# Performance work log

Hardware: AMD Instinct MI355X
Metric: run time of the kernel (lower is better)

The kernel has to match this reference:

```python
import jax, jax.numpy as jnp
import numpy as np

N = 50000      # nodes
E = 800000     # edges
G = 64         # graphs in batch
IN_F, H1, C1, C2, OUT_F = 128, 4, 32, 64, 16
D1 = H1 * C1   # 128, concat output of gat1
EPS = 1e-5
NEG_SLOPE = 0.2


def setup_inputs() -> dict:
    key = jax.random.key(0)
    ks = jax.random.split(key, 16)
    rn = lambda k, shape, s=0.1: jax.random.normal(k, shape, jnp.float32) * s
    inp = {
        'x': jax.random.normal(ks[0], (N, IN_F), jnp.float32),
        'edge_index': jax.random.randint(ks[1], (2, E), 0, N),
        'edge_attr': jax.random.uniform(ks[2], (E, 1), jnp.float32),
        'batch': jnp.sort(jax.random.randint(ks[3], (N,), 0, G)),
        # GATv2 layer 1 (heads=4, concat)
        'Wl1': rn(ks[4], (IN_F, D1)), 'bl1': jnp.zeros((D1,), jnp.float32),
        'Wr1': rn(ks[5], (IN_F, D1)), 'br1': jnp.zeros((D1,), jnp.float32),
        'We1': rn(ks[6], (1, D1)), 'att1': rn(ks[7], (H1, C1)),
        'bias1': jnp.zeros((D1,), jnp.float32),
        # GATv2 layer 2 (heads=1, concat=False)
        'Wl2': rn(ks[8], (D1, C2)), 'bl2': jnp.zeros((C2,), jnp.float32),
        'Wr2': rn(ks[9], (D1, C2)), 'br2': jnp.zeros((C2,), jnp.float32),
        'We2': rn(ks[10], (1, C2)), 'att2': rn(ks[11], (1, C2)),
        'bias2': jnp.zeros((C2,), jnp.float32),
        # batchnorms
        'bn1_gamma': jnp.ones((D1,), jnp.float32), 'bn1_beta': jnp.zeros((D1,), jnp.float32),
        'bn2_gamma': jnp.ones((C2,), jnp.float32), 'bn2_beta': jnp.zeros((C2,), jnp.float32),
        # final linear over [sum|mean|max] pooled features
        'Wlin': rn(ks[12], (3 * C2, OUT_F)), 'blin': jnp.zeros((OUT_F,), jnp.float32),
    }
    return inp


def gatv2(x, src, dst, edge_attr, Wl, bl, Wr, br, We, att, bias, H, C, concat):
    n = x.shape[0]
    xl = (x @ Wl + bl).reshape(n, H, C)          # source transform (lin_l)
    xr = (x @ Wr + br).reshape(n, H, C)          # target transform (lin_r)
    e = (edge_attr @ We).reshape(-1, H, C)       # edge transform (lin_edge)
    m = jax.nn.leaky_relu(xl[src] + xr[dst] + e, NEG_SLOPE)  # [E,H,C]
    alpha = jnp.einsum('ehc,hc->eh', m, att)     # attention logits [E,H]
    amax = jax.ops.segment_max(alpha, dst, num_segments=n)
    amax = jnp.where(jnp.isfinite(amax), amax, 0.0)
    p = jnp.exp(alpha - amax[dst])
    denom = jax.ops.segment_sum(p, dst, num_segments=n)
    a = p / (denom[dst] + 1e-16)                 # per-destination softmax
    out = jax.ops.segment_sum(xl[src] * a[:, :, None], dst, num_segments=n)
    out = out.reshape(n, H * C) if concat else out.mean(axis=1)
    return out + bias


def batchnorm(x, gamma, beta):
    mu = x.mean(axis=0)
    var = x.var(axis=0)  # biased var, as torch BN uses for normalization
    return (x - mu) * jax.lax.rsqrt(var + EPS) * gamma + beta


def reference(x, edge_index, edge_attr, batch,
              Wl1, bl1, Wr1, br1, We1, att1, bias1,
              Wl2, bl2, Wr2, br2, We2, att2, bias2,
              bn1_gamma, bn1_beta, bn2_gamma, bn2_beta,
              Wlin, blin):
    src, dst = edge_index[0], edge_index[1]
    h = jax.nn.relu(gatv2(x, src, dst, edge_attr, Wl1, bl1, Wr1, br1, We1, att1, bias1, H1, C1, True))
    h = batchnorm(h, bn1_gamma, bn1_beta)
    # dropout omitted (eval-mode reference)
    h = jax.nn.relu(gatv2(h, src, dst, edge_attr, Wl2, bl2, Wr2, br2, We2, att2, bias2, 1, C2, False))
    h = batchnorm(h, bn2_gamma, bn2_beta)
    # multi-pool over graphs
    s = jax.ops.segment_sum(h, batch, num_segments=G)
    cnt = jax.ops.segment_sum(jnp.ones((h.shape[0], 1), h.dtype), batch, num_segments=G)
    mean = s / jnp.maximum(cnt, 1.0)
    mx = jax.ops.segment_max(h, batch, num_segments=G)
    feat = jnp.concatenate([s, mean, mx], axis=-1)   # [G, 3*C2]
    return feat @ Wlin + blin
```

## Files before the change

### kernel.cpp

```cpp
#include <hip/hip_runtime.h>
#include <math.h>


typedef __attribute__((ext_vector_type(8))) short short8v;
typedef __attribute__((ext_vector_type(8))) unsigned short ushort8v;
typedef __attribute__((ext_vector_type(4))) unsigned short ushort4v;
typedef __attribute__((ext_vector_type(4))) float f32x4v;

#define BUCKCAP 8192

__device__ __forceinline__ void atomicMaxFloat(float* addr, float val) {
    if (val >= 0.f) atomicMax((int*)addr, __float_as_int(val));
    else            atomicMin((unsigned int*)addr, __float_as_uint(val));
}
__device__ __forceinline__ void atomicMinFloat(float* addr, float val) {
    if (val >= 0.f) atomicMin((int*)addr, __float_as_int(val));
    else            atomicMax((unsigned int*)addr, __float_as_uint(val));
}
__device__ __forceinline__ unsigned short f2bf(float f) {
    unsigned u = __float_as_uint(f);
    unsigned r = u + 0x7FFFu + ((u >> 16) & 1u);
    return (unsigned short)(r >> 16);
}
__device__ __forceinline__ float bf2f(unsigned short h) {
    return __uint_as_float((unsigned)h << 16);
}

__global__ __launch_bounds__(256)
void passA_kernel(const int* __restrict__ esrc_in, const int* __restrict__ edst_in,
                  const float* __restrict__ eattr,
                  const float* __restrict__ Wl1, const float* __restrict__ Wr1,
                  uint2* __restrict__ brec, int* __restrict__ bcur,
                  unsigned short* __restrict__ w1t, float* __restrict__ gsum,
                  float* __restrict__ gmax, float* __restrict__ gmin, int nE) {
    __shared__ unsigned scnt[256];
    __shared__ unsigned sbase[256];
    const int t = threadIdx.x;
    const int e0 = blockIdx.x * 1024;
    scnt[t] = 0;
    __syncthreads();
    unsigned rx[4], ry[4]; unsigned short rk[4];
#pragma unroll
    for (int j = 0; j < 4; ++j) {
        int e = e0 + j * 256 + t;
        if (e < nE) {
            unsigned d = (unsigned)edst_in[e];
            rx[j] = (d << 16) | (unsigned)esrc_in[e];
            ry[j] = __float_as_uint(eattr[e]);
            rk[j] = (unsigned short)atomicAdd(&scnt[d >> 8], 1u);
        }
    }
    __syncthreads();
    sbase[t] = (scnt[t] > 0) ? (unsigned)atomicAdd(&bcur[t], (int)scnt[t]) : 0u;
    __syncthreads();
#pragma unroll
    for (int j = 0; j < 4; ++j) {
        int e = e0 + j * 256 + t;
        if (e < nE) {
            unsigned b = rx[j] >> 24;
            unsigned pos = sbase[b] + rk[j];
            if (pos < BUCKCAP) brec[(size_t)b * BUCKCAP + pos] = make_uint2(rx[j], ry[j]);
        }
    }
    const int gid = blockIdx.x * 256 + t, gstr = gridDim.x * 256;
    for (int j = gid; j < 256 * 128; j += gstr) {
        int col = j >> 7, k = j & 127;
        float w = (col < 128) ? Wl1[k * 128 + col] : Wr1[k * 128 + (col - 128)];
        w1t[j] = f2bf(w);
    }
    for (int j = gid; j < 64 * 64; j += gstr) { gsum[j] = 0.f; gmax[j] = -INFINITY; gmin[j] = INFINITY; }
}

__global__ __launch_bounds__(256)
void passB_kernel(const uint2* __restrict__ brec, const int* __restrict__ bcur,
                  int* __restrict__ rowptr, int* __restrict__ deghist,
                  unsigned* __restrict__ edges, int nN, int nE) {
    __shared__ unsigned cnt[256];
    __shared__ int red[256];
    __shared__ int rp[256];
    __shared__ int lhist[64];
    const int b = blockIdx.x, t = threadIdx.x;
    cnt[t] = 0;
    if (t < 64) lhist[t] = 0;
    red[t] = (t < b) ? bcur[t] : 0;
    __syncthreads();
    for (int off = 128; off; off >>= 1) {
        if (t < off) red[t] += red[t + off];
        __syncthreads();
    }
    const int base = red[0];
    const int n = bcur[b];
    const uint2* r = brec + (size_t)b * BUCKCAP;
    for (int i = t; i < n; i += 256) atomicAdd(&cnt[(r[i].x >> 16) & 255u], 1u);
    __syncthreads();
    const unsigned v = cnt[t];
    const int d = (b << 8) + t;
    if (d < nN) atomicAdd(&lhist[v < 63u ? v : 63u], 1);
    red[t] = (int)v;
    __syncthreads();
    for (int off = 1; off < 256; off <<= 1) {
        int xv = (t >= off) ? red[t - off] : 0;
        __syncthreads();
        red[t] += xv;
        __syncthreads();
    }
    if (t < 64 && lhist[t] > 0) atomicAdd(&deghist[t], lhist[t]);
    rp[t] = base + red[t] - (int)v;
    if (d <= nN) rowptr[d] = rp[t];
    if (b == gridDim.x - 1 && t == 255) rowptr[nN] = nE;
    __syncthreads();
    cnt[t] = 0;
    __syncthreads();
    for (int i = t; i < n; i += 256) {
        uint2 rec = r[i];
        unsigned dlo = (rec.x >> 16) & 255u;
        unsigned rank = atomicAdd(&cnt[dlo], 1u);
        int pos = rp[dlo] + (int)rank;
        edges[pos] = (rec.x & 0xFFFFu) | ((unsigned)f2bf(__uint_as_float(rec.y)) << 16);
    }
}

template <int NO, bool F32IN, bool DOPERM>
__global__ __launch_bounds__(256)
void mfma_transform_kernel(const float* __restrict__ Af, const unsigned short* __restrict__ Ab,
                           const unsigned short* __restrict__ Wt,
                           const float* __restrict__ bL, const float* __restrict__ bR,
                           unsigned short* __restrict__ outL, unsigned short* __restrict__ outR,
                           const int* __restrict__ rowptr, const int* __restrict__ deghist,
                           int* __restrict__ bincur, unsigned short* __restrict__ perm, int M) {
    if constexpr (DOPERM) {
        if ((int)blockIdx.x < (M + 255) / 256) {
            __shared__ int gbase[64];
            __shared__ int lcnt[64];
            __shared__ int lbase[64];
            const int t = threadIdx.x;
            if (t < 64) {
                int v = deghist[t];
                int incl = v;
#pragma unroll
                for (int off = 1; off < 64; off <<= 1) {
                    int u = __shfl_up(incl, off);
                    if (t >= off) incl += u;
                }
                gbase[t] = incl - v;
                lcnt[t] = 0;
            }
            __syncthreads();
            const int dnode = blockIdx.x * 256 + t;
            int bin = 0, myrank = 0;
            if (dnode < M) {
                int deg = rowptr[dnode + 1] - rowptr[dnode];
                bin = deg < 63 ? deg : 63;
                myrank = atomicAdd(&lcnt[bin], 1);
            }
            __syncthreads();
            if (t < 64 && lcnt[t] > 0) lbase[t] = atomicAdd(&bincur[t], lcnt[t]);
            __syncthreads();
            if (dnode < M) perm[gbase[bin] + lbase[bin] + myrank] = (unsigned short)dnode;
        }
    }
    constexpr int NCG = NO / 64;
    const int wid  = (blockIdx.x * blockDim.x + threadIdx.x) >> 6;
    const int lane = threadIdx.x & 63;
    const int rowblk = wid / NCG;
    const int cg     = wid % NCG;
    if (rowblk * 16 >= M) return;
    int r = rowblk * 16 + (lane & 15);
    if (r >= M) r = M - 1;
    const int ko = (lane >> 4) * 8;
    const int cbase = cg * 64;

    f32x4v acc0 = {0.f,0.f,0.f,0.f}, acc1 = acc0, acc2 = acc0, acc3 = acc0;
#pragma unroll
    for (int k0 = 0; k0 < 128; k0 += 32) {
        short8v a;
        if constexpr (F32IN) {
            const float4 f0 = *(const float4*)(Af + (size_t)r * 128 + k0 + ko);
            const float4 f1 = *(const float4*)(Af + (size_t)r * 128 + k0 + ko + 4);
            a[0] = (short)f2bf(f0.x); a[1] = (short)f2bf(f0.y);
            a[2] = (short)f2bf(f0.z); a[3] = (short)f2bf(f0.w);
            a[4] = (short)f2bf(f1.x); a[5] = (short)f2bf(f1.y);
            a[6] = (short)f2bf(f1.z); a[7] = (short)f2bf(f1.w);
        } else {
            a = *(const short8v*)(Ab + (size_t)r * 128 + k0 + ko);
        }
        const unsigned short* wp = Wt + (size_t)(cbase + (lane & 15)) * 128 + k0 + ko;
        short8v b0 = *(const short8v*)(wp);
        short8v b1 = *(const short8v*)(wp + 16 * 128);
        short8v b2 = *(const short8v*)(wp + 32 * 128);
        short8v b3 = *(const short8v*)(wp + 48 * 128);
        acc0 = __builtin_amdgcn_mfma_f32_16x16x32_bf16(a, b0, acc0, 0, 0, 0);
        acc1 = __builtin_amdgcn_mfma_f32_16x16x32_bf16(a, b1, acc1, 0, 0, 0);
        acc2 = __builtin_amdgcn_mfma_f32_16x16x32_bf16(a, b2, acc2, 0, 0, 0);
        acc3 = __builtin_amdgcn_mfma_f32_16x16x32_bf16(a, b3, acc3, 0, 0, 0);
    }

    const int colL  = lane & 15;
    const int rquad = (lane >> 4) * 4;
    f32x4v accs[4] = { acc0, acc1, acc2, acc3 };
#pragma unroll
    for (int c = 0; c < 4; ++c) {
        const int gcol = cbase + c * 16 + colL;
        float bias; unsigned short* outp; int oc;
        if (gcol < NO / 2) { bias = bL[gcol]; outp = outL; oc = gcol; }
        else               { bias = bR[gcol - NO / 2]; outp = outR; oc = gcol - NO / 2; }
#pragma unroll
        for (int j = 0; j < 4; ++j) {
            const int row = rowblk * 16 + rquad + j;
            if (row < M) outp[(size_t)row * (NO / 2) + oc] = f2bf(accs[c][j] + bias);
        }
    }
}

__device__ __forceinline__ float edge_c8(unsigned w, bool act, ushort8v xu,
                                         const float* xrv, const float* wev,
                                         const float* atv, float* xv) {
    const float ea = bf2f((unsigned short)(w >> 16));
    float part = 0.f;
#pragma unroll
    for (int q = 0; q < 8; ++q) {
        xv[q] = bf2f(xu[q]);
        float t = xv[q] + xrv[q] + ea * wev[q];
        t = fmaxf(t, 0.2f * t);
        part += t * atv[q];
    }
    part += __shfl_xor(part, 1);
    part += __shfl_xor(part, 2);
    return act ? __expf(part) : 0.f;
}

__device__ __forceinline__ float edge_c4(unsigned w, bool act, ushort4v xu,
                                         const float* xrv, const float* wev,
                                         const float* atv, float* xv) {
    const float ea = bf2f((unsigned short)(w >> 16));
    float part = 0.f;
#pragma unroll
    for (int q = 0; q < 4; ++q) {
        xv[q] = bf2f(xu[q]);
        float t = xv[q] + xrv[q] + ea * wev[q];
        t = fmaxf(t, 0.2f * t);
        part += t * atv[q];
    }
    part += __shfl_xor(part, 1);
    part += __shfl_xor(part, 2);
    part += __shfl_xor(part, 4);
    part += __shfl_xor(part, 8);
    return act ? __expf(part) : 0.f;
}

__global__ __launch_bounds__(256)
void gather1_kernel(const unsigned short* __restrict__ xl, const unsigned short* __restrict__ xr,
                    const int* __restrict__ rowptr, const unsigned* __restrict__ edges,
                    const unsigned short* __restrict__ perm,
                    const float* __restrict__ We, const float* __restrict__ att,
                    const float* __restrict__ bias, unsigned short* __restrict__ y, int nN) {
    const int lane = threadIdx.x & 63;
    const int sub  = lane >> 4;
    const int sl   = lane & 15;
    const int c0   = sl * 8;
    const int waveg = (blockIdx.x * blockDim.x + threadIdx.x) >> 6;
    const int i = waveg * 4 + sub;
    const bool valid = (i < nN);
    const int n = valid ? (int)perm[i] : 0;

    float xrv[8];
    int ks = 0, ke = 0;
    if (valid) {
        ushort8v xu = *(const ushort8v*)(xr + (size_t)n * 128 + c0);
#pragma unroll
        for (int j = 0; j < 8; ++j) xrv[j] = bf2f(xu[j]);
        ks = rowptr[n]; ke = rowptr[n + 1];
    } else {
#pragma unroll
        for (int j = 0; j < 8; ++j) xrv[j] = 0.f;
    }
    const float4 we0 = *(const float4*)(We + c0);
    const float4 we1 = *(const float4*)(We + c0 + 4);
    const float4 at0 = *(const float4*)(att + c0);
    const float4 at1 = *(const float4*)(att + c0 + 4);
    const float wev[8] = { we0.x, we0.y, we0.z, we0.w, we1.x, we1.y, we1.z, we1.w };
    const float atv[8] = { at0.x, at0.y, at0.z, at0.w, at1.x, at1.y, at1.z, at1.w };

    float d = 0.f, a[8];
#pragma unroll
    for (int j = 0; j < 8; ++j) a[j] = 0.f;

    for (int kb = ks; __any(kb < ke); kb += 16) {
        const unsigned ew = (kb + sl < ke) ? edges[kb + sl] : 0u;
        const int cnt = ke - kb;
        for (int j = 0; j < 16; j += 4) {
            if (!__any(j < cnt)) break;
            const unsigned w0 = __shfl(ew, sub * 16 + j + 0);
            const unsigned w1 = __shfl(ew, sub * 16 + j + 1);
            const unsigned w2 = __shfl(ew, sub * 16 + j + 2);
            const unsigned w3 = __shfl(ew, sub * 16 + j + 3);
            const ushort8v xu0 = *(const ushort8v*)(xl + (size_t)(w0 & 0xFFFFu) * 128 + c0);
            const ushort8v xu1 = *(const ushort8v*)(xl + (size_t)(w1 & 0xFFFFu) * 128 + c0);
            const ushort8v xu2 = *(const ushort8v*)(xl + (size_t)(w2 & 0xFFFFu) * 128 + c0);
            const ushort8v xu3 = *(const ushort8v*)(xl + (size_t)(w3 & 0xFFFFu) * 128 + c0);
            float xva[8], xvb[8];
            const float e0 = edge_c8(w0, j + 0 < cnt, xu0, xrv, wev, atv, xva);
            const float e1 = edge_c8(w1, j + 1 < cnt, xu1, xrv, wev, atv, xvb);
            d += e0 + e1;
#pragma unroll
            for (int q = 0; q < 8; ++q) a[q] += e0 * xva[q] + e1 * xvb[q];
            const float e2 = edge_c8(w2, j + 2 < cnt, xu2, xrv, wev, atv, xva);
            const float e3 = edge_c8(w3, j + 3 < cnt, xu3, xrv, wev, atv, xvb);
            d += e2 + e3;
#pragma unroll
            for (int q = 0; q < 8; ++q) a[q] += e2 * xva[q] + e3 * xvb[q];
        }
    }
    if (valid) {
        const float inv = 1.f / (d + 1e-16f);
        ushort8v o;
#pragma unroll
        for (int j = 0; j < 8; ++j) o[j] = f2bf(fmaxf(a[j] * inv + bias[c0 + j], 0.f));
        *(ushort8v*)(y + (size_t)n * 128 + c0) = o;
    }
}

__global__ __launch_bounds__(256)
void gather2_kernel(const unsigned short* __restrict__ xl, const unsigned short* __restrict__ xr,
                    const int* __restrict__ rowptr, const unsigned* __restrict__ edges,
                    const unsigned short* __restrict__ perm,
                    const float* __restrict__ We, const float* __restrict__ att,
                    const float* __restrict__ bias, float* __restrict__ y, int nN) {
    const int lane = threadIdx.x & 63;
    const int sub  = lane >> 4;
    const int sl   = lane & 15;
    const int c0   = sl * 4;
    const int waveg = (blockIdx.x * blockDim.x + threadIdx.x) >> 6;
    const int i = waveg * 4 + sub;
    const bool valid = (i < nN);
    const int n = valid ? (int)perm[i] : 0;

    float xrv[4];
    int ks = 0, ke = 0;
    if (valid) {
        ushort4v xu = *(const ushort4v*)(xr + (size_t)n * 64 + c0);
#pragma unroll
        for (int j = 0; j < 4; ++j) xrv[j] = bf2f(xu[j]);
        ks = rowptr[n]; ke = rowptr[n + 1];
    } else {
#pragma unroll
        for (int j = 0; j < 4; ++j) xrv[j] = 0.f;
    }
    const float4 wev4 = *(const float4*)(We + c0);
    const float4 atv4 = *(const float4*)(att + c0);
    const float wev[4] = { wev4.x, wev4.y, wev4.z, wev4.w };
    const float atv[4] = { atv4.x, atv4.y, atv4.z, atv4.w };

    float d = 0.f, a[4] = {0.f, 0.f, 0.f, 0.f};
    for (int kb = ks; __any(kb < ke); kb += 16) {
        const unsigned ew = (kb + sl < ke) ? edges[kb + sl] : 0u;
        const int cnt = ke - kb;
        for (int j = 0; j < 16; j += 4) {
            if (!__any(j < cnt)) break;
            const unsigned w0 = __shfl(ew, sub * 16 + j + 0);
            const unsigned w1 = __shfl(ew, sub * 16 + j + 1);
            const unsigned w2 = __shfl(ew, sub * 16 + j + 2);
            const unsigned w3 = __shfl(ew, sub * 16 + j + 3);
            const ushort4v xu0 = *(const ushort4v*)(xl + (size_t)(w0 & 0xFFFFu) * 64 + c0);
            const ushort4v xu1 = *(const ushort4v*)(xl + (size_t)(w1 & 0xFFFFu) * 64 + c0);
            const ushort4v xu2 = *(const ushort4v*)(xl + (size_t)(w2 & 0xFFFFu) * 64 + c0);
            const ushort4v xu3 = *(const ushort4v*)(xl + (size_t)(w3 & 0xFFFFu) * 64 + c0);
            float xva[4], xvb[4];
            const float e0 = edge_c4(w0, j + 0 < cnt, xu0, xrv, wev, atv, xva);
            const float e1 = edge_c4(w1, j + 1 < cnt, xu1, xrv, wev, atv, xvb);
            d += e0 + e1;
#pragma unroll
            for (int q = 0; q < 4; ++q) a[q] += e0 * xva[q] + e1 * xvb[q];
            const float e2 = edge_c4(w2, j + 2 < cnt, xu2, xrv, wev, atv, xva);
            const float e3 = edge_c4(w3, j + 3 < cnt, xu3, xrv, wev, atv, xvb);
            d += e2 + e3;
#pragma unroll
            for (int q = 0; q < 4; ++q) a[q] += e2 * xva[q] + e3 * xvb[q];
        }
    }
    if (valid) {
        const float inv = 1.f / (d + 1e-16f);
        float4 o;
        o.x = fmaxf(a[0] * inv + bias[c0],     0.f);
        o.y = fmaxf(a[1] * inv + bias[c0 + 1], 0.f);
        o.z = fmaxf(a[2] * inv + bias[c0 + 2], 0.f);
        o.w = fmaxf(a[3] * inv + bias[c0 + 3], 0.f);
        *(float4*)(y + (size_t)n * 64 + c0) = o;
    }
}

__global__ void bn_stats_bf128_kernel(const unsigned short* __restrict__ y,
                                      float* __restrict__ stats, int rows) {
    const int t = threadIdx.x;
    const int col = t & 127;
    const int rsub = t >> 7;
    float s = 0.f, q = 0.f;
    for (int r = blockIdx.x * 2 + rsub; r < rows; r += gridDim.x * 2) {
        float v = bf2f(y[(size_t)r * 128 + col]);
        s += v; q += v * v;
    }
    atomicAdd(&stats[col], s);
    atomicAdd(&stats[128 + col], q);
}

__global__ void wfold2_kernel(const float* __restrict__ Wl2, const float* __restrict__ bl2,
                              const float* __restrict__ Wr2, const float* __restrict__ br2,
                              const float* __restrict__ stats, const float* __restrict__ gamma,
                              const float* __restrict__ beta,
                              unsigned short* __restrict__ w2t, float* __restrict__ b2f, int nN) {
    __shared__ float sc[128], sh[128];
    const int t = threadIdx.x;
    if (t < 128) {
        float invN = 1.f / nN;
        float mu = stats[t] * invN;
        float var = stats[128 + t] * invN - mu * mu;
        float k = gamma[t] * rsqrtf(var + 1e-5f);
        sc[t] = k; sh[t] = beta[t] - mu * k;
    }
    __syncthreads();
    if (t < 128) {
        const int oc = (t < 64) ? t : t - 64;
        const float* W = (t < 64) ? Wl2 : Wr2;
        float acc = (t < 64) ? bl2[oc] : br2[oc];
        for (int k = 0; k < 128; ++k) acc += sh[k] * W[k * 64 + oc];
        b2f[t] = acc;
    }
    for (int i = t; i < 128 * 128; i += 256) {
        int col = i >> 7, k = i & 127;
        const int oc = (col < 64) ? col : col - 64;
        const float* W = (col < 64) ? Wl2 : Wr2;
        w2t[i] = f2bf(sc[k] * W[k * 64 + oc]);
    }
}

__global__ void pool_kernel(const float* __restrict__ y2, const int* __restrict__ batch,
                            float* __restrict__ gsum, float* __restrict__ gmax,
                            float* __restrict__ gmin, float* __restrict__ gcnt,
                            float* __restrict__ bn2stats, int rows) {
    const int t = threadIdx.x;
    const int col = t & 63;
    const int rsub = t >> 6;
    const int base = blockIdx.x * 256;
    int curg = -1; float s = 0.f, mx = 0.f, mn = 0.f, cnt = 0.f;
    float bs = 0.f, bq = 0.f;
    int rend = rows < base + 256 ? rows : base + 256;
    for (int r = base + rsub; r < rend; r += 4) {
        int g = batch[r];
        float v = y2[(size_t)r * 64 + col];
        bs += v; bq += v * v;
        if (g != curg) {
            if (curg >= 0) {
                atomicAdd(&gsum[curg * 64 + col], s);
                atomicMaxFloat(&gmax[curg * 64 + col], mx);
                atomicMinFloat(&gmin[curg * 64 + col], mn);
                if (col == 0) atomicAdd(&gcnt[curg], cnt);
            }
            curg = g; s = v; mx = v; mn = v; cnt = 1.f;
        } else {
            s += v; mx = fmaxf(mx, v); mn = fminf(mn, v); cnt += 1.f;
        }
    }
    if (curg >= 0) {
        atomicAdd(&gsum[curg * 64 + col], s);
        atomicMaxFloat(&gmax[curg * 64 + col], mx);
        atomicMinFloat(&gmin[curg * 64 + col], mn);
        if (col == 0) atomicAdd(&gcnt[curg], cnt);
    }
    __shared__ float red[2][4][64];
    red[0][rsub][col] = bs; red[1][rsub][col] = bq;
    __syncthreads();
    if (rsub == 0) {
        float ts = red[0][0][col] + red[0][1][col] + red[0][2][col] + red[0][3][col];
        float tq = red[1][0][col] + red[1][1][col] + red[1][2][col] + red[1][3][col];
        atomicAdd(&bn2stats[col], ts);
        atomicAdd(&bn2stats[64 + col], tq);
    }
}

__global__ void final_kernel(const float* __restrict__ gsum, const float* __restrict__ gmax,
                             const float* __restrict__ gmin, const float* __restrict__ gcnt,
                             const float* __restrict__ bn2stats, const float* __restrict__ gamma,
                             const float* __restrict__ beta, const float* __restrict__ Wlin,
                             const float* __restrict__ blin, float* __restrict__ out, int nN) {
    __shared__ float feat[64][192];
    __shared__ float sc[64], sh[64];
    int t = threadIdx.x;
    if (t < 64) {
        float invN = 1.f / nN;
        float mu = bn2stats[t] * invN;
        float var = bn2stats[64 + t] * invN - mu * mu;
        float k = gamma[t] * rsqrtf(var + 1e-5f);
        sc[t] = k; sh[t] = beta[t] - mu * k;
    }
    __syncthreads();
    for (int i = t; i < 64 * 64; i += 256) {
        int g = i >> 6, c = i & 63;
        float cntg = gcnt[g];
        float s_bn = sc[c] * gsum[i] + sh[c] * cntg;
        feat[g][c]       = s_bn;
        feat[g][64 + c]  = s_bn / fmaxf(cntg, 1.f);
        feat[g][128 + c] = (sc[c] >= 0.f) ? sc[c] * gmax[i] + sh[c]
                                          : sc[c] * gmin[i] + sh[c];
    }
    __syncthreads();
    for (int i = t; i < 64 * 16; i += 256) {
        int g = i >> 4, j = i & 15;
        float acc = blin[j];
        for (int k = 0; k < 192; ++k) acc += feat[g][k] * Wlin[k * 16 + j];
        out[g * 16 + j] = acc;
    }
}

extern "C" void kernel_launch(void* const* d_in, const int* in_sizes, int n_in,
                              void* d_out, int out_size, void* d_ws, size_t ws_size,
                              hipStream_t stream) {
    const float* x     = (const float*)d_in[0];
    const int*   eidx  = (const int*)d_in[1];
    const float* eattr = (const float*)d_in[2];
    const int*   batch = (const int*)d_in[3];
    const float* Wl1 = (const float*)d_in[4];  const float* bl1 = (const float*)d_in[5];
    const float* Wr1 = (const float*)d_in[6];  const float* br1 = (const float*)d_in[7];
    const float* We1 = (const float*)d_in[8];  const float* att1 = (const float*)d_in[9];
    const float* bias1 = (const float*)d_in[10];
    const float* Wl2 = (const float*)d_in[11]; const float* bl2 = (const float*)d_in[12];
    const float* Wr2 = (const float*)d_in[13]; const float* br2 = (const float*)d_in[14];
    const float* We2 = (const float*)d_in[15]; const float* att2 = (const float*)d_in[16];
    const float* bias2 = (const float*)d_in[17];
    const float* g1 = (const float*)d_in[18];  const float* b1 = (const float*)d_in[19];
    const float* g2 = (const float*)d_in[20];  const float* b2 = (const float*)d_in[21];
    const float* Wlin = (const float*)d_in[22]; const float* blin = (const float*)d_in[23];
    float* out = (float*)d_out;

    const int nN = in_sizes[0] / 128;
    const int nE = in_sizes[1] / 2;
    const int* esrc_in = eidx;
    const int* edst_in = eidx + nE;
    const int nbuck = (nN + 255) >> 8;

    char* ws = (char*)d_ws;
    size_t o = 0;
    auto alloc = [&](size_t bytes) { size_t r = o; o += (bytes + 255) & ~(size_t)255; return r; };
    unsigned short* B0 = (unsigned short*)(ws + alloc((size_t)nN * 128 * 2));
    unsigned short* B1 = (unsigned short*)(ws + alloc((size_t)nN * 128 * 2));
    char*           B2 = (char*)(ws + alloc((size_t)nN * 128 * 2));
    unsigned short* w1t = (unsigned short*)(ws + alloc(256 * 128 * 2));
    unsigned short* w2t = (unsigned short*)(ws + alloc(128 * 128 * 2));
    float* b2f    = (float*)(ws + alloc(128 * 4));
    uint2* brec   = (uint2*)(ws + alloc((size_t)nbuck * BUCKCAP * 8));
    unsigned* edges = (unsigned*)(ws + alloc((size_t)nE * 4));
    int* ctrl = (int*)(ws + alloc(832 * 4));
    int*   bcur     = ctrl;
    int*   deghist  = ctrl + 256;
    int*   bincur   = ctrl + 320;
    float* bn1stats = (float*)(ctrl + 384);
    float* bn2stats = (float*)(ctrl + 640);
    float* gcnt     = (float*)(ctrl + 768);
    int*   rowptr = (int*)(ws + alloc((size_t)(nN + 1) * 4));
    unsigned short* perm = (unsigned short*)(ws + alloc((size_t)nN * 2));
    float* gsum = (float*)(ws + alloc(64 * 64 * 4));
    float* gmax = (float*)(ws + alloc(64 * 64 * 4));
    float* gmin = (float*)(ws + alloc(64 * 64 * 4));

    unsigned short* y1bf = B0;
    unsigned short* xl1b = B1;
    unsigned short* xr1b = (unsigned short*)B2;
    unsigned short* xl2b = B1;
    unsigned short* xr2b = B1 + (size_t)nN * 64;
    float*          y2   = (float*)B2;

    const int mBlk = (nN + 15) / 16;
    const int t1Blocks = mBlk;
    const int t2Blocks = (mBlk * 2 + 3) / 4;

    hipMemsetAsync(ctrl, 0, 832 * 4, stream);
    passA_kernel<<<(nE + 1023) / 1024, 256, 0, stream>>>(
        esrc_in, edst_in, eattr, Wl1, Wr1, brec, bcur, w1t, gsum, gmax, gmin, nE);
    passB_kernel<<<nbuck, 256, 0, stream>>>(brec, bcur, rowptr, deghist, edges, nN, nE);

    mfma_transform_kernel<256, true, true><<<t1Blocks, 256, 0, stream>>>(
        x, nullptr, w1t, bl1, br1, xl1b, xr1b, rowptr, deghist, bincur, perm, nN);
    gather1_kernel<<<(nN + 15) / 16, 256, 0, stream>>>(
        xl1b, xr1b, rowptr, edges, perm, We1, att1, bias1, y1bf, nN);
    bn_stats_bf128_kernel<<<256, 256, 0, stream>>>(y1bf, bn1stats, nN);
    wfold2_kernel<<<1, 256, 0, stream>>>(Wl2, bl2, Wr2, br2, bn1stats, g1, b1, w2t, b2f, nN);

    mfma_transform_kernel<128, false, false><<<t2Blocks, 256, 0, stream>>>(
        nullptr, y1bf, w2t, b2f, b2f + 64, xl2b, xr2b, nullptr, nullptr, nullptr, nullptr, nN);
    gather2_kernel<<<(nN + 15) / 16, 256, 0, stream>>>(
        xl2b, xr2b, rowptr, edges, perm, We2, att2, bias2, y2, nN);

    pool_kernel<<<(nN + 255) / 256, 256, 0, stream>>>(y2, batch, gsum, gmax, gmin, gcnt, bn2stats, nN);
    final_kernel<<<1, 256, 0, stream>>>(gsum, gmax, gmin, gcnt, bn2stats, g2, b2, Wlin, blin, out, nN);
}
```

Before: 368.3 us.

## Stage transform weights in LDS and run persistent tiles with register prefetch

The MFMA linear-transform kernel now copies the whole transposed weight matrix into padded LDS once per block. It then loops persistently over 32-row tiles, staging each activation tile through LDS and prefetching the next tile's rows into registers while computing the current one. This is meant to cut the repeated global or L2 weight fetches that every wave used to make, and to overlap input loads with MFMA work. The cost is a large LDS footprint (about 78 KB for the first layer), which limits occupancy, plus fixed grid sizes and extra block-wide barriers per tile.

```diff
diff --git a/kernel.cpp b/kernel.cpp
--- a/kernel.cpp
+++ b/kernel.cpp
@@ -8,6 +8,7 @@
 typedef __attribute__((ext_vector_type(4))) float f32x4v;
 
 #define BUCKCAP 8192
+#define WS 136
 
 __device__ __forceinline__ void atomicMaxFloat(float* addr, float val) {
     if (val >= 0.f) atomicMax((int*)addr, __float_as_int(val));
@@ -128,12 +129,15 @@
                            unsigned short* __restrict__ outL, unsigned short* __restrict__ outR,
                            const int* __restrict__ rowptr, const int* __restrict__ deghist,
                            int* __restrict__ bincur, unsigned short* __restrict__ perm, int M) {
+    __shared__ unsigned short wlds[NO * WS];
+    __shared__ unsigned short alds[32 * WS];
+    const int t = threadIdx.x;
+
     if constexpr (DOPERM) {
         if ((int)blockIdx.x < (M + 255) / 256) {
-            __shared__ int gbase[64];
-            __shared__ int lcnt[64];
-            __shared__ int lbase[64];
-            const int t = threadIdx.x;
+            int* gbase = (int*)alds;
+            int* lcnt  = gbase + 64;
+            int* lbase = gbase + 128;
             if (t < 64) {
                 int v = deghist[t];
                 int incl = v;
@@ -159,55 +163,129 @@
             if (dnode < M) perm[gbase[bin] + lbase[bin] + myrank] = (unsigned short)dnode;
         }
     }
-    constexpr int NCG = NO / 64;
-    const int wid  = (blockIdx.x * blockDim.x + threadIdx.x) >> 6;
-    const int lane = threadIdx.x & 63;
-    const int rowblk = wid / NCG;
-    const int cg     = wid % NCG;
-    if (rowblk * 16 >= M) return;
-    int r = rowblk * 16 + (lane & 15);
-    if (r >= M) r = M - 1;
-    const int ko = (lane >> 4) * 8;
-    const int cbase = cg * 64;
-
-    f32x4v acc0 = {0.f,0.f,0.f,0.f}, acc1 = acc0, acc2 = acc0, acc3 = acc0;
-#pragma unroll
-    for (int k0 = 0; k0 < 128; k0 += 32) {
-        short8v a;
+
+    for (int i = t; i < NO * 16; i += 256) {
+        int c = i >> 4, seg = (i & 15) * 8;
+        *(ushort8v*)&wlds[c * WS + seg] = *(const ushort8v*)&Wt[c * 128 + seg];
+    }
+
+    const int wave = t >> 6, lane = t & 63;
+    const int colL = lane & 15;
+    const int ko   = (lane >> 4) * 8;
+    const int rquad = (lane >> 4) * 4;
+    const int arow = t >> 3;
+    const int acol = (t & 7) * 16;
+    const int nTiles = (M + 31) / 32;
+
+    float4   pf[4];
+    ushort8v pb[2];
+    int tile = blockIdx.x;
+    if (tile < nTiles) {
+        int g = tile * 32 + arow; if (g >= M) g = M - 1;
         if constexpr (F32IN) {
-            const float4 f0 = *(const float4*)(Af + (size_t)r * 128 + k0 + ko);
-            const float4 f1 = *(const float4*)(Af + (size_t)r * 128 + k0 + ko + 4);
-            a[0] = (short)f2bf(f0.x); a[1] = (short)f2bf(f0.y);
-            a[2] = (short)f2bf(f0.z); a[3] = (short)f2bf(f0.w);
-            a[4] = (short)f2bf(f1.x); a[5] = (short)f2bf(f1.y);
-            a[6] = (short)f2bf(f1.z); a[7] = (short)f2bf(f1.w);
+#pragma unroll
+            for (int q = 0; q < 4; ++q) pf[q] = *(const float4*)(Af + (size_t)g * 128 + acol + q * 4);
         } else {
-            a = *(const short8v*)(Ab + (size_t)r * 128 + k0 + ko);
-        }
-        const unsigned short* wp = Wt + (size_t)(cbase + (lane & 15)) * 128 + k0 + ko;
-        short8v b0 = *(const short8v*)(wp);
-        short8v b1 = *(const short8v*)(wp + 16 * 128);
-        short8v b2 = *(const short8v*)(wp + 32 * 128);
-        short8v b3 = *(const short8v*)(wp + 48 * 128);
-        acc0 = __builtin_amdgcn_mfma_f32_16x16x32_bf16(a, b0, acc0, 0, 0, 0);
-        acc1 = __builtin_amdgcn_mfma_f32_16x16x32_bf16(a, b1, acc1, 0, 0, 0);
-        acc2 = __builtin_amdgcn_mfma_f32_16x16x32_bf16(a, b2, acc2, 0, 0, 0);
-        acc3 = __builtin_amdgcn_mfma_f32_16x16x32_bf16(a, b3, acc3, 0, 0, 0);
-    }
-
-    const int colL  = lane & 15;
-    const int rquad = (lane >> 4) * 4;
-    f32x4v accs[4] = { acc0, acc1, acc2, acc3 };
-#pragma unroll
-    for (int c = 0; c < 4; ++c) {
-        const int gcol = cbase + c * 16 + colL;
-        float bias; unsigned short* outp; int oc;
-        if (gcol < NO / 2) { bias = bL[gcol]; outp = outL; oc = gcol; }
-        else               { bias = bR[gcol - NO / 2]; outp = outR; oc = gcol - NO / 2; }
-#pragma unroll
-        for (int j = 0; j < 4; ++j) {
-            const int row = rowblk * 16 + rquad + j;
-            if (row < M) outp[(size_t)row * (NO / 2) + oc] = f2bf(accs[c][j] + bias);
+#pragma unroll
+            for (int q = 0; q < 2; ++q) pb[q] = *(const ushort8v*)(Ab + (size_t)g * 128 + acol + q * 8);
+        }
+    }
+
+    for (; tile < nTiles; tile += gridDim.x) {
+        __syncthreads();
+        if constexpr (F32IN) {
+#pragma unroll
+            for (int q = 0; q < 2; ++q) {
+                ushort8v o;
+                o[0] = f2bf(pf[2*q].x);   o[1] = f2bf(pf[2*q].y);
+                o[2] = f2bf(pf[2*q].z);   o[3] = f2bf(pf[2*q].w);
+                o[4] = f2bf(pf[2*q+1].x); o[5] = f2bf(pf[2*q+1].y);
+                o[6] = f2bf(pf[2*q+1].z); o[7] = f2bf(pf[2*q+1].w);
+                *(ushort8v*)&alds[arow * WS + acol + q * 8] = o;
+            }
+        } else {
+#pragma unroll
+            for (int q = 0; q < 2; ++q) *(ushort8v*)&alds[arow * WS + acol + q * 8] = pb[q];
+        }
+        __syncthreads();
+
+        const int nexttile = tile + gridDim.x;
+        if (nexttile < nTiles) {
+            int g = nexttile * 32 + arow; if (g >= M) g = M - 1;
+            if constexpr (F32IN) {
+#pragma unroll
+                for (int q = 0; q < 4; ++q) pf[q] = *(const float4*)(Af + (size_t)g * 128 + acol + q * 4);
+            } else {
+#pragma unroll
+                for (int q = 0; q < 2; ++q) pb[q] = *(const ushort8v*)(Ab + (size_t)g * 128 + acol + q * 8);
+            }
+        }
+
+        if constexpr (NO == 256) {
+            f32x4v acc[2][4];
+#pragma unroll
+            for (int rb = 0; rb < 2; ++rb)
+#pragma unroll
+                for (int c = 0; c < 4; ++c) acc[rb][c] = f32x4v{0.f,0.f,0.f,0.f};
+#pragma unroll
+            for (int k0 = 0; k0 < 128; k0 += 32) {
+                short8v b0 = *(const short8v*)&wlds[(wave * 64 +  0 + colL) * WS + k0 + ko];
+                short8v b1 = *(const short8v*)&wlds[(wave * 64 + 16 + colL) * WS + k0 + ko];
+                short8v b2 = *(const short8v*)&wlds[(wave * 64 + 32 + colL) * WS + k0 + ko];
+                short8v b3 = *(const short8v*)&wlds[(wave * 64 + 48 + colL) * WS + k0 + ko];
+#pragma unroll
+                for (int rb = 0; rb < 2; ++rb) {
+                    short8v a = *(const short8v*)&alds[(rb * 16 + colL) * WS + k0 + ko];
+                    acc[rb][0] = __builtin_amdgcn_mfma_f32_16x16x32_bf16(a, b0, acc[rb][0], 0, 0, 0);
+                    acc[rb][1] = __builtin_amdgcn_mfma_f32_16x16x32_bf16(a, b1, acc[rb][1], 0, 0, 0);
+                    acc[rb][2] = __builtin_amdgcn_mfma_f32_16x16x32_bf16(a, b2, acc[rb][2], 0, 0, 0);
+                    acc[rb][3] = __builtin_amdgcn_mfma_f32_16x16x32_bf16(a, b3, acc[rb][3], 0, 0, 0);
+                }
+            }
+#pragma unroll
+            for (int rb = 0; rb < 2; ++rb)
+#pragma unroll
+            for (int c = 0; c < 4; ++c) {
+                const int gcol = wave * 64 + c * 16 + colL;
+                float bias; unsigned short* outp; int oc;
+                if (gcol < 128) { bias = bL[gcol]; outp = outL; oc = gcol; }
+                else            { bias = bR[gcol - 128]; outp = outR; oc = gcol - 128; }
+#pragma unroll
+                for (int j = 0; j < 4; ++j) {
+                    const int row = tile * 32 + rb * 16 + rquad + j;
+                    if (row < M) outp[(size_t)row * 128 + oc] = f2bf(acc[rb][c][j] + bias);
+                }
+            }
+        } else {
+            const int cg = wave & 1;
+            const int rsub = (wave >> 1) * 16;
+            f32x4v acc[4];
+#pragma unroll
+            for (int c = 0; c < 4; ++c) acc[c] = f32x4v{0.f,0.f,0.f,0.f};
+#pragma unroll
+            for (int k0 = 0; k0 < 128; k0 += 32) {
+                short8v a  = *(const short8v*)&alds[(rsub + colL) * WS + k0 + ko];
+                short8v b0 = *(const short8v*)&wlds[(cg * 64 +  0 + colL) * WS + k0 + ko];
+                short8v b1 = *(const short8v*)&wlds[(cg * 64 + 16 + colL) * WS + k0 + ko];
+                short8v b2 = *(const short8v*)&wlds[(cg * 64 + 32 + colL) * WS + k0 + ko];
+                short8v b3 = *(const short8v*)&wlds[(cg * 64 + 48 + colL) * WS + k0 + ko];
+                acc[0] = __builtin_amdgcn_mfma_f32_16x16x32_bf16(a, b0, acc[0], 0, 0, 0);
+                acc[1] = __builtin_amdgcn_mfma_f32_16x16x32_bf16(a, b1, acc[1], 0, 0, 0);
+                acc[2] = __builtin_amdgcn_mfma_f32_16x16x32_bf16(a, b2, acc[2], 0, 0, 0);
+                acc[3] = __builtin_amdgcn_mfma_f32_16x16x32_bf16(a, b3, acc[3], 0, 0, 0);
+            }
+#pragma unroll
+            for (int c = 0; c < 4; ++c) {
+                const int gcol = cg * 64 + c * 16 + colL;
+                float bias; unsigned short* outp; int oc;
+                if (gcol < 64) { bias = bL[gcol]; outp = outL; oc = gcol; }
+                else           { bias = bR[gcol - 64]; outp = outR; oc = gcol - 64; }
+#pragma unroll
+                for (int j = 0; j < 4; ++j) {
+                    const int row = tile * 32 + rsub + rquad + j;
+                    if (row < M) outp[(size_t)row * 64 + oc] = f2bf(acc[c][j] + bias);
+                }
+            }
         }
     }
 }
@@ -568,23 +646,19 @@
     unsigned short* xr2b = B1 + (size_t)nN * 64;
     float*          y2   = (float*)B2;
 
-    const int mBlk = (nN + 15) / 16;
-    const int t1Blocks = mBlk;
-    const int t2Blocks = (mBlk * 2 + 3) / 4;
-
     hipMemsetAsync(ctrl, 0, 832 * 4, stream);
     passA_kernel<<<(nE + 1023) / 1024, 256, 0, stream>>>(
         esrc_in, edst_in, eattr, Wl1, Wr1, brec, bcur, w1t, gsum, gmax, gmin, nE);
     passB_kernel<<<nbuck, 256, 0, stream>>>(brec, bcur, rowptr, deghist, edges, nN, nE);
 
-    mfma_transform_kernel<256, true, true><<<t1Blocks, 256, 0, stream>>>(
+    mfma_transform_kernel<256, true, true><<<512, 256, 0, stream>>>(
         x, nullptr, w1t, bl1, br1, xl1b, xr1b, rowptr, deghist, bincur, perm, nN);
     gather1_kernel<<<(nN + 15) / 16, 256, 0, stream>>>(
         xl1b, xr1b, rowptr, edges, perm, We1, att1, bias1, y1bf, nN);
     bn_stats_bf128_kernel<<<256, 256, 0, stream>>>(y1bf, bn1stats, nN);
     wfold2_kernel<<<1, 256, 0, stream>>>(Wl2, bl2, Wr2, br2, bn1stats, g1, b1, w2t, b2f, nN);
 
-    mfma_transform_kernel<128, false, false><<<t2Blocks, 256, 0, stream>>>(
+    mfma_transform_kernel<128, false, false><<<768, 256, 0, stream>>>(
         nullptr, y1bf, w2t, b2f, b2f + 64, xl2b, xr2b, nullptr, nullptr, nullptr, nullptr, nN);
     gather2_kernel<<<(nN + 15) / 16, 256, 0, stream>>>(
         xl2b, xr2b, rowptr, edges, perm, We2, att2, bias2, y2, nN);
```

Result: faster. 338.5 us (-8.1%).
